# Kernel optimization log

Hardware: AMD Instinct MI355X
Metric: run time of the kernel (lower is better)

The kernel has to match this reference:

```python
import jax, jax.numpy as jnp
import numpy as np
from jax import lax

IMG_SIZE = 512        # efficientdet-d0 input resolution
TOP_K = 256           # fixed candidate count for jit-compatible NMS
THRESHOLD = 0.01      # score threshold (init kwarg)
IOU_THRESHOLD = 0.5   # NMS IoU threshold (init kwarg)


def make_anchors():
    """Standard EfficientDet-d0 anchors: P3-P7, 3 scales x 3 ratios, xyxy."""
    strides = [8, 16, 32, 64, 128]
    scales = [2.0 ** 0, 2.0 ** (1.0 / 3.0), 2.0 ** (2.0 / 3.0)]
    ratios = [0.5, 1.0, 2.0]
    base = 4.0
    out = []
    for s in strides:
        fs = IMG_SIZE // s
        xs = (np.arange(fs, dtype=np.float32) + 0.5) * s
        cy, cx = np.meshgrid(xs, xs, indexing='ij')
        for r in ratios:
            for sc in scales:
                w = base * s * sc * np.sqrt(1.0 / r)
                h = base * s * sc * np.sqrt(r)
                a = np.stack([cx - w / 2, cy - h / 2, cx + w / 2, cy + h / 2], -1)
                out.append(a.reshape(-1, 4))
    return np.concatenate(out, 0).astype(np.float32)  # [49104, 4]


def decode_boxes(anchors, regs):
    """RetinaNet-style delta decode. anchors [A,4] xyxy, regs [B,A,4]."""
    aw = anchors[:, 2] - anchors[:, 0]
    ah = anchors[:, 3] - anchors[:, 1]
    acx = anchors[:, 0] + 0.5 * aw
    acy = anchors[:, 1] + 0.5 * ah
    dx, dy, dw, dh = regs[..., 0], regs[..., 1], regs[..., 2], regs[..., 3]
    cx = acx + dx * aw
    cy = acy + dy * ah
    w = aw * jnp.exp(jnp.clip(dw, -4.0, 4.0))
    h = ah * jnp.exp(jnp.clip(dh, -4.0, 4.0))
    boxes = jnp.stack([cx - 0.5 * w, cy - 0.5 * h, cx + 0.5 * w, cy + 0.5 * h], -1)
    return jnp.clip(boxes, 0.0, float(IMG_SIZE))  # [B,A,4]


def pairwise_iou(boxes):
    """boxes [K,4] xyxy -> iou [K,K]."""
    area = jnp.maximum(boxes[:, 2] - boxes[:, 0], 0) * jnp.maximum(boxes[:, 3] - boxes[:, 1], 0)
    lt = jnp.maximum(boxes[:, None, :2], boxes[None, :, :2])
    rb = jnp.minimum(boxes[:, None, 2:], boxes[None, :, 2:])
    wh = jnp.maximum(rb - lt, 0.0)
    inter = wh[..., 0] * wh[..., 1]
    union = area[:, None] + area[None, :] - inter
    return inter / jnp.maximum(union, 1e-8)


def nms_keep(boxes, scores):
    """Sequential NMS over score-sorted candidates. boxes [K,4], scores [K]."""
    K = boxes.shape[0]
    iou = pairwise_iou(boxes)  # [K,K]
    ar = jnp.arange(K)
    keep0 = scores > 0.0

    def body(i, keep):
        suppressed = jnp.any(keep & (iou[:, i] > IOU_THRESHOLD) & (ar < i))
        return keep.at[i].set(keep[i] & ~suppressed)

    return lax.fori_loop(0, K, body, keep0)


def setup_inputs() -> dict:
    key = jax.random.key(0)
    k1, k2 = jax.random.split(key)
    B, A, C = 8, 49104, 80
    cls_logits = jax.random.normal(k1, (B, A, C), dtype=jnp.float32) - 2.0
    box_regs = 0.2 * jax.random.normal(k2, (B, A, 4), dtype=jnp.float32)
    anchors = jnp.asarray(make_anchors())
    return {"cls_logits": cls_logits, "box_regs": box_regs, "anchors": anchors}


def reference(cls_logits, box_regs, anchors):
    probs = jax.nn.sigmoid(cls_logits)            # [B,A,C]
    scores = probs.max(-1)                        # [B,A]
    labels = probs.argmax(-1)                     # [B,A]
    boxes = decode_boxes(anchors, box_regs)       # [B,A,4]
    scores = jnp.where(scores > THRESHOLD, scores, 0.0)
    top_s, idx = lax.top_k(scores, TOP_K)         # [B,K]
    top_b = jnp.take_along_axis(boxes, idx[..., None], axis=1)   # [B,K,4]
    top_l = jnp.take_along_axis(labels, idx, axis=1)             # [B,K]
    keep = jax.vmap(nms_keep)(top_b, top_s)                      # [B,K] bool
    keep_f = keep.astype(top_b.dtype)
    dets = jnp.concatenate([top_b * keep_f[..., None], (top_s * keep_f)[..., None]], -1)  # [B,K,5]
    return dets, top_l, keep
```

## Files before the change

kernel.cpp:

```cpp
#include <hip/hip_runtime.h>
#include <stdint.h>
#include <math.h>

#define IMGF   512.0f
#define A_N    49104
#define B_N    8
#define C_N    80
#define K_N    256
#define IOU_T  0.5f
#define NBIN   16384
#define HSHIFT 16
#define CAP    2048

__global__ __launch_bounds__(256) void score_kernel(
    const float* __restrict__ logits,
    uint32_t* __restrict__ keys,
    int* __restrict__ labels)
{
    const int tid  = threadIdx.x;
    const int wave = tid >> 6, lane = tid & 63;
    const int grp  = lane >> 2, j = lane & 3;
    const int g0 = blockIdx.x * 128 + wave * 32 + grp;

    const float4* p0 = (const float4*)(logits + (size_t)g0 * C_N);
    const float4* p1 = (const float4*)(logits + (size_t)(g0 + 16) * C_N);
    unsigned long long best0 = 0ull, best1 = 0ull;
#pragma unroll
    for (int k = 0; k < 5; ++k) {
        float4 v0 = p0[j + 4 * k];
        float4 v1 = p1[j + 4 * k];
        const int bl = (j + 4 * k) * 4;
        float a0[4] = { v0.x, v0.y, v0.z, v0.w };
        float a1[4] = { v1.x, v1.y, v1.z, v1.w };
#pragma unroll
        for (int q = 0; q < 4; ++q) {
            uint32_t b0 = __float_as_uint(a0[q]);
            uint32_t u0 = b0 ^ (0x80000000u | (uint32_t)((int32_t)b0 >> 31));
            unsigned long long pk0 = ((unsigned long long)u0 << 32)
                                   | (uint32_t)(~(uint32_t)(bl + q));
            if (pk0 > best0) best0 = pk0;
            uint32_t b1 = __float_as_uint(a1[q]);
            uint32_t u1 = b1 ^ (0x80000000u | (uint32_t)((int32_t)b1 >> 31));
            unsigned long long pk1 = ((unsigned long long)u1 << 32)
                                   | (uint32_t)(~(uint32_t)(bl + q));
            if (pk1 > best1) best1 = pk1;
        }
    }
    {
        unsigned long long o;
        o = __shfl_xor(best0, 1, 64); if (o > best0) best0 = o;
        o = __shfl_xor(best0, 2, 64); if (o > best0) best0 = o;
        o = __shfl_xor(best1, 1, 64); if (o > best1) best1 = o;
        o = __shfl_xor(best1, 2, 64); if (o > best1) best1 = o;
    }
    if (j == 0) {
        uint32_t u0  = (uint32_t)(best0 >> 32);
        uint32_t mb0 = (u0 & 0x80000000u) ? (u0 ^ 0x80000000u) : ~u0;
        float m0 = __uint_as_float(mb0);
        float s0 = 1.0f / (1.0f + expf(-m0));
        if (!(s0 > 0.01f)) s0 = 0.0f;
        keys[g0]   = __float_as_uint(s0);
        labels[g0] = (int)~((uint32_t)best0);

        uint32_t u1  = (uint32_t)(best1 >> 32);
        uint32_t mb1 = (u1 & 0x80000000u) ? (u1 ^ 0x80000000u) : ~u1;
        float m1 = __uint_as_float(mb1);
        float s1 = 1.0f / (1.0f + expf(-m1));
        if (!(s1 > 0.01f)) s1 = 0.0f;
        keys[g0 + 16]   = __float_as_uint(s1);
        labels[g0 + 16] = (int)~((uint32_t)best1);
    }
}

__global__ __launch_bounds__(1024) void select_nms_kernel(
    const uint32_t* __restrict__ keys,
    const int* __restrict__ labels,
    const float* __restrict__ regs,
    const float* __restrict__ anchors,
    float* __restrict__ out)
{
    const int b   = blockIdx.x;
    const int tid = threadIdx.x;

    __shared__ uint32_t hist[NBIN];
    __shared__ int ssum[1024];
    __shared__ int sh_T, sh_nc;
    __shared__ unsigned long long cand[CAP];
    __shared__ unsigned long long sorted[K_N];
    __shared__ float4 sbox[K_N];
    __shared__ float  sscore[K_N];
    __shared__ int    slab[K_N];
    __shared__ unsigned long long supr[K_N][4];
    __shared__ unsigned long long keepw[4];

    const uint32_t* kb = keys + (size_t)b * A_N;
    const uint4* kb4 = (const uint4*)kb;
    const int N4 = A_N / 4;

    for (int i = tid; i < NBIN; i += 1024) hist[i] = 0;
    __syncthreads();
    for (int i = tid; i < N4; i += 1024) {
        uint4 v = kb4[i];
        atomicAdd(&hist[v.x >> HSHIFT], 1u);
        atomicAdd(&hist[v.y >> HSHIFT], 1u);
        atomicAdd(&hist[v.z >> HSHIFT], 1u);
        atomicAdd(&hist[v.w >> HSHIFT], 1u);
    }
    __syncthreads();

    const int lo = tid * (NBIN / 1024);
    int seg = 0;
#pragma unroll
    for (int q = 0; q < NBIN / 1024; ++q) seg += (int)hist[lo + q];
    ssum[tid] = seg;
    __syncthreads();
    for (int off = 1; off < 1024; off <<= 1) {
        int v = (tid + off < 1024) ? ssum[tid + off] : 0;
        __syncthreads();
        ssum[tid] += v;
        __syncthreads();
    }
    int above = ssum[tid] - seg;
    if (above < K_N && above + seg >= K_N) {
        int cum = above;
        for (int bin = lo + NBIN / 1024 - 1; bin >= lo; --bin) {
            int c = (int)hist[bin];
            if (cum + c >= K_N) { sh_T = bin; break; }
            cum += c;
        }
    }
    if (tid == 0) sh_nc = 0;
    __syncthreads();
    const uint32_t T = (uint32_t)sh_T;

    for (int i = tid; i < N4; i += 1024) {
        uint4 v = kb4[i];
        uint32_t ks[4] = { v.x, v.y, v.z, v.w };
#pragma unroll
        for (int q = 0; q < 4; ++q) {
            if ((ks[q] >> HSHIFT) >= T) {
                int p = atomicAdd(&sh_nc, 1);
                if (p < CAP)
                    cand[p] = ((unsigned long long)ks[q] << 32)
                            | (unsigned long long)(0xFFFFFFFFu - (uint32_t)(4 * i + q));
            }
        }
    }
    if (tid < K_N) sorted[tid] = 0ull;
    __syncthreads();
    int nc = sh_nc; if (nc > CAP) nc = CAP;

    for (int i = tid; i < nc; i += 1024) {
        unsigned long long me = cand[i];
        int r = 0;
        for (int jq = 0; jq < nc; ++jq) r += (cand[jq] > me);
        if (r < K_N) sorted[r] = me;
    }
    __syncthreads();

    if (tid < K_N) {
#pragma clang fp contract(off)
        unsigned long long cv = sorted[tid];
        uint32_t key = (uint32_t)(cv >> 32);
        uint32_t ai  = 0xFFFFFFFFu - (uint32_t)cv;
        if (ai >= (uint32_t)A_N) ai = 0;
        int a = (int)ai;
        float s = __uint_as_float(key);
        sscore[tid] = s;
        slab[tid]   = labels[(size_t)b * A_N + a];

        float ax0 = anchors[4 * a + 0], ay0 = anchors[4 * a + 1];
        float ax1 = anchors[4 * a + 2], ay1 = anchors[4 * a + 3];
        float aw = ax1 - ax0, ah = ay1 - ay0;
        float acx = ax0 + 0.5f * aw, acy = ay0 + 0.5f * ah;
        const float* r = regs + ((size_t)b * A_N + a) * 4;
        float dx = r[0], dy = r[1], dw = r[2], dh = r[3];
        float cx = acx + dx * aw;
        float cy = acy + dy * ah;
        dw = fminf(fmaxf(dw, -4.0f), 4.0f);
        dh = fminf(fmaxf(dh, -4.0f), 4.0f);
        float w = aw * expf(dw);
        float h = ah * expf(dh);
        float x0 = cx - 0.5f * w, y0 = cy - 0.5f * h;
        float x1 = cx + 0.5f * w, y1 = cy + 0.5f * h;
        x0 = fminf(fmaxf(x0, 0.0f), IMGF);
        y0 = fminf(fmaxf(y0, 0.0f), IMGF);
        x1 = fminf(fmaxf(x1, 0.0f), IMGF);
        y1 = fminf(fmaxf(y1, 0.0f), IMGF);
        sbox[tid] = make_float4(x0, y0, x1, y1);
    }
    __syncthreads();

    {
#pragma clang fp contract(off)
        const int row = tid & 255, gq = tid >> 8;
        float4 bi = sbox[row];
        float areai = fmaxf(bi.z - bi.x, 0.0f) * fmaxf(bi.w - bi.y, 0.0f);
        unsigned long long m = 0;
        const int jlo = gq * 64, jhi = jlo + 64;
        int start = row + 1 > jlo ? row + 1 : jlo;
        for (int jx = start; jx < jhi; ++jx) {
            float4 bj = sbox[jx];
            float areaj = fmaxf(bj.z - bj.x, 0.0f) * fmaxf(bj.w - bj.y, 0.0f);
            float lx = fmaxf(bi.x, bj.x), ly = fmaxf(bi.y, bj.y);
            float rx = fminf(bi.z, bj.z), ry = fminf(bi.w, bj.w);
            float iw = fmaxf(rx - lx, 0.0f), ih = fmaxf(ry - ly, 0.0f);
            float inter = iw * ih;
            float uni = areai + areaj - inter;
            float iou = inter / fmaxf(uni, 1e-8f);
            if (iou > IOU_T) m |= 1ull << (jx & 63);
        }
        supr[row][gq] = m;
    }
    if (tid < K_N) {
        unsigned long long ball = __ballot(sscore[tid] > 0.0f);
        if ((tid & 63) == 0) keepw[tid >> 6] = ball;
    }
    __syncthreads();

    if (tid == 0) {
        unsigned long long k0 = keepw[0], k1 = keepw[1], k2 = keepw[2], k3 = keepw[3];
#define NMS_CHUNK(c, kc)                                                     \
        for (int l = 0; l < 64; ++l) {                                       \
            const int i = (c) * 64 + l;                                      \
            unsigned long long w0 = supr[i][0], w1 = supr[i][1];             \
            unsigned long long w2 = supr[i][2], w3 = supr[i][3];             \
            if ((kc >> l) & 1ull) {                                          \
                k0 &= ~w0; k1 &= ~w1; k2 &= ~w2; k3 &= ~w3;                  \
            }                                                                \
        }
        NMS_CHUNK(0, k0)
        NMS_CHUNK(1, k1)
        NMS_CHUNK(2, k2)
        NMS_CHUNK(3, k3)
#undef NMS_CHUNK
        keepw[0] = k0; keepw[1] = k1; keepw[2] = k2; keepw[3] = k3;
    }
    __syncthreads();

    if (tid < K_N) {
        float keepf = ((keepw[tid >> 6] >> (tid & 63)) & 1ull) ? 1.0f : 0.0f;
        float4 bx = sbox[tid];
        float s = sscore[tid];
        float* det = out + ((size_t)b * K_N + tid) * 5;
        det[0] = bx.x * keepf;
        det[1] = bx.y * keepf;
        det[2] = bx.z * keepf;
        det[3] = bx.w * keepf;
        det[4] = s * keepf;
        out[(size_t)B_N * K_N * 5 + (size_t)b * K_N + tid] = (float)slab[tid];
        out[(size_t)B_N * K_N * 5 + (size_t)B_N * K_N + (size_t)b * K_N + tid] = keepf;
    }
}

extern "C" void kernel_launch(void* const* d_in, const int* in_sizes, int n_in,
                              void* d_out, int out_size, void* d_ws, size_t ws_size,
                              hipStream_t stream)
{
    const float* logits  = (const float*)d_in[0];
    const float* regs    = (const float*)d_in[1];
    const float* anchors = (const float*)d_in[2];
    float* out = (float*)d_out;

    uint32_t* keys   = (uint32_t*)d_ws;
    int*      labels = (int*)(keys + (size_t)B_N * A_N);

    const int total = B_N * A_N;
    score_kernel<<<total / 128, 256, 0, stream>>>(logits, keys, labels);
    select_nms_kernel<<<B_N, 1024, 0, stream>>>(keys, labels, regs, anchors, out);
}
```

Before: 239.5 us.

## Use persistent grid-stride score kernel with prefetch and linear-value histogram bins

The score kernel becomes a persistent grid-stride loop over 768 blocks. Each 4-lane group handles a pair of adjacent rows and software-prefetches the next pair's logits into registers while it reduces the current pair. The packed 64-bit max/argmax compare is replaced with an fmaxf reduction followed by a first-index-of-max pass. The histogram binning switches from the top 16 bits of the float key to a linear bucketing of the score value, which spreads the scores near the top-k threshold across more bins and should leave fewer candidates to rank. The costs are higher register pressure from the double buffers and a second pass to find the argmax.

```diff
diff --git a/kernel.cpp b/kernel.cpp
--- a/kernel.cpp
+++ b/kernel.cpp
@@ -9,8 +9,14 @@
 #define K_N    256
 #define IOU_T  0.5f
 #define NBIN   16384
-#define HSHIFT 16
 #define CAP    2048
+#define NPAIR  (B_N * A_N / 2)
+
+__device__ __forceinline__ int bin_of(uint32_t key) {
+    float s = __uint_as_float(key);
+    int b = (int)(s * 16384.0f);
+    return b > 16383 ? 16383 : b;
+}
 
 __global__ __launch_bounds__(256) void score_kernel(
     const float* __restrict__ logits,
@@ -18,57 +24,68 @@
     int* __restrict__ labels)
 {
     const int tid  = threadIdx.x;
-    const int wave = tid >> 6, lane = tid & 63;
+    const int lane = tid & 63;
     const int grp  = lane >> 2, j = lane & 3;
-    const int g0 = blockIdx.x * 128 + wave * 32 + grp;
-
-    const float4* p0 = (const float4*)(logits + (size_t)g0 * C_N);
-    const float4* p1 = (const float4*)(logits + (size_t)(g0 + 16) * C_N);
-    unsigned long long best0 = 0ull, best1 = 0ull;
-#pragma unroll
-    for (int k = 0; k < 5; ++k) {
-        float4 v0 = p0[j + 4 * k];
-        float4 v1 = p1[j + 4 * k];
-        const int bl = (j + 4 * k) * 4;
-        float a0[4] = { v0.x, v0.y, v0.z, v0.w };
-        float a1[4] = { v1.x, v1.y, v1.z, v1.w };
-#pragma unroll
-        for (int q = 0; q < 4; ++q) {
-            uint32_t b0 = __float_as_uint(a0[q]);
-            uint32_t u0 = b0 ^ (0x80000000u | (uint32_t)((int32_t)b0 >> 31));
-            unsigned long long pk0 = ((unsigned long long)u0 << 32)
-                                   | (uint32_t)(~(uint32_t)(bl + q));
-            if (pk0 > best0) best0 = pk0;
-            uint32_t b1 = __float_as_uint(a1[q]);
-            uint32_t u1 = b1 ^ (0x80000000u | (uint32_t)((int32_t)b1 >> 31));
-            unsigned long long pk1 = ((unsigned long long)u1 << 32)
-                                   | (uint32_t)(~(uint32_t)(bl + q));
-            if (pk1 > best1) best1 = pk1;
-        }
-    }
+    const int ggid = blockIdx.x * 64 + (tid >> 6) * 16 + grp;
+    const int NGt  = gridDim.x * 64;
+
+    float4 c[10];
+    int p = ggid;
     {
-        unsigned long long o;
-        o = __shfl_xor(best0, 1, 64); if (o > best0) best0 = o;
-        o = __shfl_xor(best0, 2, 64); if (o > best0) best0 = o;
-        o = __shfl_xor(best1, 1, 64); if (o > best1) best1 = o;
-        o = __shfl_xor(best1, 2, 64); if (o > best1) best1 = o;
-    }
-    if (j == 0) {
-        uint32_t u0  = (uint32_t)(best0 >> 32);
-        uint32_t mb0 = (u0 & 0x80000000u) ? (u0 ^ 0x80000000u) : ~u0;
-        float m0 = __uint_as_float(mb0);
-        float s0 = 1.0f / (1.0f + expf(-m0));
-        if (!(s0 > 0.01f)) s0 = 0.0f;
-        keys[g0]   = __float_as_uint(s0);
-        labels[g0] = (int)~((uint32_t)best0);
-
-        uint32_t u1  = (uint32_t)(best1 >> 32);
-        uint32_t mb1 = (u1 & 0x80000000u) ? (u1 ^ 0x80000000u) : ~u1;
-        float m1 = __uint_as_float(mb1);
-        float s1 = 1.0f / (1.0f + expf(-m1));
-        if (!(s1 > 0.01f)) s1 = 0.0f;
-        keys[g0 + 16]   = __float_as_uint(s1);
-        labels[g0 + 16] = (int)~((uint32_t)best1);
+        const float4* r = (const float4*)(logits + (size_t)(2 * p) * C_N);
+#pragma unroll
+        for (int k = 0; k < 5; ++k) { c[k] = r[j + 4 * k]; c[5 + k] = r[20 + j + 4 * k]; }
+    }
+    while (true) {
+        const int pn = p + NGt;
+        const bool vn = pn < NPAIR;
+        float4 n[10];
+        if (vn) {
+            const float4* r = (const float4*)(logits + (size_t)(2 * pn) * C_N);
+#pragma unroll
+            for (int k = 0; k < 5; ++k) { n[k] = r[j + 4 * k]; n[5 + k] = r[20 + j + 4 * k]; }
+        }
+        {
+            const float* f = (const float*)c;
+            float m0 = f[0], m1 = f[20];
+#pragma unroll
+            for (int q = 1; q < 20; ++q) m0 = fmaxf(m0, f[q]);
+#pragma unroll
+            for (int q = 1; q < 20; ++q) m1 = fmaxf(m1, f[20 + q]);
+            m0 = fmaxf(m0, __shfl_xor(m0, 1, 64));
+            m0 = fmaxf(m0, __shfl_xor(m0, 2, 64));
+            m1 = fmaxf(m1, __shfl_xor(m1, 1, 64));
+            m1 = fmaxf(m1, __shfl_xor(m1, 2, 64));
+            int cl0 = 1 << 30, cl1 = 1 << 30;
+#pragma unroll
+            for (int k = 0; k < 5; ++k) {
+#pragma unroll
+                for (int q = 0; q < 4; ++q) {
+                    const int cc = (j + 4 * k) * 4 + q;
+                    const float v0 = ((const float*)&c[k])[q];
+                    const float v1 = ((const float*)&c[5 + k])[q];
+                    if (v0 == m0 && cc < cl0) cl0 = cc;
+                    if (v1 == m1 && cc < cl1) cl1 = cc;
+                }
+            }
+            { int t = __shfl_xor(cl0, 1, 64); if (t < cl0) cl0 = t;
+              t = __shfl_xor(cl0, 2, 64); if (t < cl0) cl0 = t; }
+            { int t = __shfl_xor(cl1, 1, 64); if (t < cl1) cl1 = t;
+              t = __shfl_xor(cl1, 2, 64); if (t < cl1) cl1 = t; }
+            if (j < 2) {
+                const float m = (j == 0) ? m0 : m1;
+                const int  cl = (j == 0) ? cl0 : cl1;
+                float s = 1.0f / (1.0f + expf(-m));
+                if (!(s > 0.01f)) s = 0.0f;
+                const int row = 2 * p + j;
+                keys[row]   = __float_as_uint(s);
+                labels[row] = cl;
+            }
+        }
+        if (!vn) break;
+#pragma unroll
+        for (int q = 0; q < 10; ++q) c[q] = n[q];
+        p = pn;
     }
 }
 
@@ -101,10 +118,10 @@
     __syncthreads();
     for (int i = tid; i < N4; i += 1024) {
         uint4 v = kb4[i];
-        atomicAdd(&hist[v.x >> HSHIFT], 1u);
-        atomicAdd(&hist[v.y >> HSHIFT], 1u);
-        atomicAdd(&hist[v.z >> HSHIFT], 1u);
-        atomicAdd(&hist[v.w >> HSHIFT], 1u);
+        atomicAdd(&hist[bin_of(v.x)], 1u);
+        atomicAdd(&hist[bin_of(v.y)], 1u);
+        atomicAdd(&hist[bin_of(v.z)], 1u);
+        atomicAdd(&hist[bin_of(v.w)], 1u);
     }
     __syncthreads();
 
@@ -131,14 +148,14 @@
     }
     if (tid == 0) sh_nc = 0;
     __syncthreads();
-    const uint32_t T = (uint32_t)sh_T;
+    const int T = sh_T;
 
     for (int i = tid; i < N4; i += 1024) {
         uint4 v = kb4[i];
         uint32_t ks[4] = { v.x, v.y, v.z, v.w };
 #pragma unroll
         for (int q = 0; q < 4; ++q) {
-            if ((ks[q] >> HSHIFT) >= T) {
+            if (bin_of(ks[q]) >= T) {
                 int p = atomicAdd(&sh_nc, 1);
                 if (p < CAP)
                     cand[p] = ((unsigned long long)ks[q] << 32)
@@ -265,7 +282,6 @@
     uint32_t* keys   = (uint32_t*)d_ws;
     int*      labels = (int*)(keys + (size_t)B_N * A_N);
 
-    const int total = B_N * A_N;
-    score_kernel<<<total / 128, 256, 0, stream>>>(logits, keys, labels);
+    score_kernel<<<768, 256, 0, stream>>>(logits, keys, labels);
     select_nms_kernel<<<B_N, 1024, 0, stream>>>(keys, labels, regs, anchors, out);
 }
```

Result: no change. 239.7 us (+0.1%).
